# Kernel tuning notes

Hardware: AMD Instinct MI355X
Metric: run time of the kernel (lower is better)

Reference implementation:

```python
import jax, jax.numpy as jnp
import numpy as np

DIM = 4096
KROT = 8
GROUP = 128
NG = DIM // GROUP  # 32 groups
N = 16384          # tokens


def setup_inputs() -> dict:
    key = jax.random.key(0)
    kx, kt, ks = jax.random.split(key, 3)
    x = jax.random.normal(kx, (N, DIM), dtype=jnp.float32)
    theta = jax.random.normal(kt, (KROT, DIM // 2), dtype=jnp.float32) * 0.1
    # pairs: for each krot layer, a permutation of [0, GROUP) tiled across groups
    rng = np.random.default_rng(0)
    pairs = np.stack([
        np.tile(rng.permutation(GROUP).astype(np.int32), NG) for _ in range(KROT)
    ])  # [KROT, DIM], local (within-group) indices
    channel_scales = jax.random.uniform(ks, (1, DIM), dtype=jnp.float32,
                                        minval=0.5, maxval=1.5)
    return {"x": x, "pairs": jnp.asarray(pairs), "theta": theta,
            "channel_scales": channel_scales}


def reference(x, pairs, theta, channel_scales):
    # global channel offset for each position of the tiled permutation
    off = jnp.repeat(jnp.arange(NG, dtype=jnp.int32) * GROUP, GROUP)  # [DIM]
    for k in range(KROT):
        idx = pairs[k] + off          # [DIM] global channel indices (a permutation)
        ie = idx[0::2]                # [DIM//2] first element of each Givens pair
        io = idx[1::2]                # [DIM//2] second element
        a = x[:, ie]                  # [N, DIM//2]
        b = x[:, io]
        c = jnp.cos(theta[k])         # [DIM//2]
        s = jnp.sin(theta[k])
        x = x.at[:, ie].set(a * c - b * s).at[:, io].set(a * s + b * c)
    return x * channel_scales
```

## Files before the change

kernel.cpp:

```cpp
#include <hip/hip_runtime.h>
#include <hip/hip_bf16.h>

#define DIMX  4096
#define KROT  8
#define GRP   128
#define NGG   32
#define NROWS 16384
#define RTILE 128
#define NRT   (NROWS / RTILE)
#define PBLK  16

typedef float f32x4 __attribute__((ext_vector_type(4)));
typedef short s16x8 __attribute__((ext_vector_type(8)));
typedef unsigned short u16;

__global__ __launch_bounds__(512) void compose(const float* __restrict__ theta,
                                               const int*   __restrict__ pairs,
                                               const float* __restrict__ scales,
                                               u16* __restrict__ B) {
    __shared__ float M[GRP * GRP];
    const int g = blockIdx.x;
    const int tid = threadIdx.x;
    const int j = tid & 127, q = tid >> 7;

    for (int r = q * 32; r < q * 32 + 32; ++r) M[r * GRP + j] = (r == j) ? 1.f : 0.f;
    __syncthreads();

    for (int k = 0; k < KROT; ++k) {
        for (int t = 0; t < 16; ++t) {
            int tp = q * 16 + t;
            int ie = pairs[k * DIMX + g * GRP + 2 * tp];
            int io = pairs[k * DIMX + g * GRP + 2 * tp + 1];
            float ang = theta[k * (DIMX / 2) + g * 64 + tp];
            float c = cosf(ang), s = sinf(ang);
            float a = M[ie * GRP + j], b = M[io * GRP + j];
            M[ie * GRP + j] = a * c - b * s;
            M[io * GRP + j] = a * s + b * c;
        }
        __syncthreads();
    }

    const int l = tid & 63, nt = (tid >> 6) & 1, ks = (tid >> 7) & 3;
    for (int w = 0; w < 4; ++w) {
        int c = w * 32 + nt * 16 + (l & 15);
        float sc = scales[g * GRP + c];
        int dbase = ks * 32 + ((l >> 4) & 3) * 8;
        s16x8 vh, vl;
        #pragma unroll
        for (int e = 0; e < 8; ++e) {
            float v = sc * M[c * GRP + dbase + e];
            __hip_bfloat16 h = __float2bfloat16(v);
            float r = v - __bfloat162float(h);
            __hip_bfloat16 lo = __float2bfloat16(r);
            vh[e] = (short)*(u16*)&h;
            vl[e] = (short)*(u16*)&lo;
        }
        int off = (((g * 4 + w) * 4 + ks) * 2 + nt) * 2;
        *(s16x8*)(B + (size_t)(off + 0) * 512 + l * 8) = vh;
        *(s16x8*)(B + (size_t)(off + 1) * 512 + l * 8) = vl;
    }
}

__global__ __launch_bounds__(256, 2) void rot_gemm(const float* __restrict__ x,
                                                   const u16* __restrict__ B,
                                                   float* __restrict__ out) {
    __shared__ float At[RTILE * GRP];
    const int tid = threadIdx.x;
    const int l = tid & 63, wv = tid >> 6;
    const int g = blockIdx.x >> 4;
    const int p = blockIdx.x & (PBLK - 1);

    s16x8 bh[4][2], bl[4][2];
    #pragma unroll
    for (int ks = 0; ks < 4; ++ks)
        #pragma unroll
        for (int nt = 0; nt < 2; ++nt) {
            int off = (((g * 4 + wv) * 4 + ks) * 2 + nt) * 2;
            bh[ks][nt] = *(const s16x8*)(B + (size_t)(off + 0) * 512 + l * 8);
            bl[ks][nt] = *(const s16x8*)(B + (size_t)(off + 1) * 512 + l * 8);
        }

    for (int t = p; t < NRT; t += PBLK) {
        const float* xb = x + (size_t)t * RTILE * DIMX + g * GRP;

        #pragma unroll
        for (int i = 0; i < 16; ++i) {
            int Lb = i * 256 + tid;
            int row = Lb >> 5, blk = Lb & 31;
            const float* src = xb + (size_t)row * DIMX + ((blk ^ (row & 7)) * 4);
            float* dst = &At[(i * 256 + wv * 64) * 4];
            __builtin_amdgcn_global_load_lds(
                (const __attribute__((address_space(1))) void*)src,
                (__attribute__((address_space(3))) void*)dst, 16, 0, 0);
        }
        __syncthreads();

        f32x4 acc[8][2] = {};
        #pragma unroll
        for (int ks = 0; ks < 4; ++ks) {
            #pragma unroll
            for (int m = 0; m < 8; ++m) {
                int row = m * 16 + (l & 15);
                int bb = ks * 8 + ((l >> 4) & 3) * 2;
                const f32x4* lp = (const f32x4*)At;
                f32x4 a0 = lp[row * 32 + ((bb)     ^ (row & 7))];
                f32x4 a1 = lp[row * 32 + ((bb + 1) ^ (row & 7))];
                s16x8 ah, al;
                #pragma unroll
                for (int e = 0; e < 8; ++e) {
                    float v = (e < 4) ? a0[e] : a1[e - 4];
                    __hip_bfloat16 h = __float2bfloat16(v);
                    float rr = v - __bfloat162float(h);
                    __hip_bfloat16 lo = __float2bfloat16(rr);
                    ah[e] = (short)*(u16*)&h;
                    al[e] = (short)*(u16*)&lo;
                }
                #pragma unroll
                for (int nt = 0; nt < 2; ++nt) {
                    acc[m][nt] = __builtin_amdgcn_mfma_f32_16x16x32_bf16(ah, bh[ks][nt], acc[m][nt], 0, 0, 0);
                    acc[m][nt] = __builtin_amdgcn_mfma_f32_16x16x32_bf16(ah, bl[ks][nt], acc[m][nt], 0, 0, 0);
                    acc[m][nt] = __builtin_amdgcn_mfma_f32_16x16x32_bf16(al, bh[ks][nt], acc[m][nt], 0, 0, 0);
                }
            }
        }
        __syncthreads();

        float* ob = out + (size_t)t * RTILE * DIMX + g * GRP + wv * 32;
        #pragma unroll
        for (int m = 0; m < 8; ++m)
            #pragma unroll
            for (int nt = 0; nt < 2; ++nt)
                #pragma unroll
                for (int i = 0; i < 4; ++i) {
                    int row = m * 16 + ((l >> 4) & 3) * 4 + i;
                    ob[(size_t)row * DIMX + nt * 16 + (l & 15)] = acc[m][nt][i];
                }
    }
}

extern "C" void kernel_launch(void* const* d_in, const int* in_sizes, int n_in,
                              void* d_out, int out_size, void* d_ws, size_t ws_size,
                              hipStream_t stream) {
    const float* xin    = (const float*)d_in[0];
    const int*   pairs  = (const int*)d_in[1];
    const float* theta  = (const float*)d_in[2];
    const float* scales = (const float*)d_in[3];
    float* outp = (float*)d_out;
    u16*   Btab = (u16*)d_ws;

    compose<<<NGG, 512, 0, stream>>>(theta, pairs, scales, Btab);
    rot_gemm<<<NGG * PBLK, 256, 0, stream>>>(xin, Btab, outp);
}
```

Measured before the change: 544.4 us.

## Load x directly into registers and stage output through swizzled LDS for coalesced stores

```diff
diff --git a/kernel.cpp b/kernel.cpp
--- a/kernel.cpp
+++ b/kernel.cpp
@@ -6,9 +6,10 @@
 #define GRP   128
 #define NGG   32
 #define NROWS 16384
-#define RTILE 128
-#define NRT   (NROWS / RTILE)
-#define PBLK  16
+#define RT2   64
+#define NT2   (NROWS / RT2)
+#define GPG   24
+#define GRID2 (NGG * GPG)
 
 typedef float f32x4 __attribute__((ext_vector_type(4)));
 typedef short s16x8 __attribute__((ext_vector_type(8)));
@@ -61,14 +62,15 @@
     }
 }
 
-__global__ __launch_bounds__(256, 2) void rot_gemm(const float* __restrict__ x,
+__global__ __launch_bounds__(256, 3) void rot_gemm(const float* __restrict__ x,
                                                    const u16* __restrict__ B,
                                                    float* __restrict__ out) {
-    __shared__ float At[RTILE * GRP];
+    __shared__ __align__(16) float C[RT2 * GRP];
     const int tid = threadIdx.x;
-    const int l = tid & 63, wv = tid >> 6;
-    const int g = blockIdx.x >> 4;
-    const int p = blockIdx.x & (PBLK - 1);
+    const int l  = tid & 63, wv = tid >> 6;
+    const int lr = l & 15;
+    const int lq = (l >> 4) & 3;
+    const int g  = blockIdx.x & 31;
 
     s16x8 bh[4][2], bl[4][2];
     #pragma unroll
@@ -80,39 +82,29 @@
             bl[ks][nt] = *(const s16x8*)(B + (size_t)(off + 1) * 512 + l * 8);
         }
 
-    for (int t = p; t < NRT; t += PBLK) {
-        const float* xb = x + (size_t)t * RTILE * DIMX + g * GRP;
+    for (int rt = blockIdx.x >> 5; rt < NT2; rt += GPG) {
+        const float* xt = x + (size_t)(rt * RT2) * DIMX + g * GRP;
+        f32x4 acc[4][2] = {};
 
-        #pragma unroll
-        for (int i = 0; i < 16; ++i) {
-            int Lb = i * 256 + tid;
-            int row = Lb >> 5, blk = Lb & 31;
-            const float* src = xb + (size_t)row * DIMX + ((blk ^ (row & 7)) * 4);
-            float* dst = &At[(i * 256 + wv * 64) * 4];
-            __builtin_amdgcn_global_load_lds(
-                (const __attribute__((address_space(1))) void*)src,
-                (__attribute__((address_space(3))) void*)dst, 16, 0, 0);
-        }
-        __syncthreads();
-
-        f32x4 acc[8][2] = {};
-        #pragma unroll
-        for (int ks = 0; ks < 4; ++ks) {
+        #pragma unroll 1
+        for (int m = 0; m < 4; ++m) {
+            f32x4 a0[4], a1[4];
             #pragma unroll
-            for (int m = 0; m < 8; ++m) {
-                int row = m * 16 + (l & 15);
-                int bb = ks * 8 + ((l >> 4) & 3) * 2;
-                const f32x4* lp = (const f32x4*)At;
-                f32x4 a0 = lp[row * 32 + ((bb)     ^ (row & 7))];
-                f32x4 a1 = lp[row * 32 + ((bb + 1) ^ (row & 7))];
+            for (int ks = 0; ks < 4; ++ks) {
+                const float* p = xt + (size_t)(m * 16 + lr) * DIMX + ks * 32 + lq * 8;
+                a0[ks] = *(const f32x4*)p;
+                a1[ks] = *(const f32x4*)(p + 4);
+            }
+            #pragma unroll
+            for (int ks = 0; ks < 4; ++ks) {
                 s16x8 ah, al;
                 #pragma unroll
                 for (int e = 0; e < 8; ++e) {
-                    float v = (e < 4) ? a0[e] : a1[e - 4];
-                    __hip_bfloat16 h = __float2bfloat16(v);
-                    float rr = v - __bfloat162float(h);
-                    __hip_bfloat16 lo = __float2bfloat16(rr);
-                    ah[e] = (short)*(u16*)&h;
+                    float v = (e < 4) ? a0[ks][e] : a1[ks][e - 4];
+                    unsigned u = __builtin_bit_cast(unsigned, v);
+                    ah[e] = (short)(u >> 16);
+                    float r = v - __builtin_bit_cast(float, u & 0xffff0000u);
+                    __hip_bfloat16 lo = __float2bfloat16(r);
                     al[e] = (short)*(u16*)&lo;
                 }
                 #pragma unroll
@@ -123,18 +115,28 @@
                 }
             }
         }
-        __syncthreads();
 
-        float* ob = out + (size_t)t * RTILE * DIMX + g * GRP + wv * 32;
         #pragma unroll
-        for (int m = 0; m < 8; ++m)
+        for (int m = 0; m < 4; ++m)
             #pragma unroll
             for (int nt = 0; nt < 2; ++nt)
                 #pragma unroll
                 for (int i = 0; i < 4; ++i) {
-                    int row = m * 16 + ((l >> 4) & 3) * 4 + i;
-                    ob[(size_t)row * DIMX + nt * 16 + (l & 15)] = acc[m][nt][i];
+                    int row = m * 16 + lq * 4 + i;
+                    int col = wv * 32 + nt * 16 + lr;
+                    C[row * GRP + (col ^ ((row & 12) << 2))] = acc[m][nt][i];
                 }
+        __syncthreads();
+
+        float* ob = out + (size_t)(rt * RT2) * DIMX + g * GRP;
+        #pragma unroll
+        for (int j = 0; j < 8; ++j) {
+            int flat = j * 256 + tid;
+            int row = flat >> 5, c4 = (flat & 31) * 4;
+            f32x4 v = *(const f32x4*)&C[row * GRP + (c4 ^ ((row & 12) << 2))];
+            *(f32x4*)(ob + (size_t)row * DIMX + c4) = v;
+        }
+        __syncthreads();
     }
 }
 
@@ -149,5 +151,5 @@
     u16*   Btab = (u16*)d_ws;
 
     compose<<<NGG, 512, 0, stream>>>(theta, pairs, scales, Btab);
-    rot_gemm<<<NGG * PBLK, 256, 0, stream>>>(xin, Btab, outp);
+    rot_gemm<<<GRID2, 256, 0, stream>>>(xin, Btab, outp);
 }
```

Result: faster. 508.2 us (-6.7%).
